# Performance work log

Measured on AMD Instinct MI355X. Metric: run time of the kernel, lower is better.

Reference implementation:

```python
import jax, jax.numpy as jnp
import numpy as np
from jax import lax

B, C, N = 8, 3, 65536
NUM_POINTS = 1024


def setup_inputs() -> dict:
    key = jax.random.key(0)
    points = jax.random.normal(key, (B, C, N), dtype=jnp.float32)
    return {"points": points}


def furthest_point_sampling(xyz, num_points):
    # xyz: (B, N, 3) -> indices (B, num_points), int32
    b, n, _ = xyz.shape
    init_idx = jnp.zeros((b,), dtype=jnp.int32)  # CUDA FPS seeds with index 0
    init_dists = jnp.full((b, n), 1e10, dtype=xyz.dtype)

    def step(carry, _):
        dists, last_idx = carry
        last_pt = jnp.take_along_axis(xyz, last_idx[:, None, None], axis=1)  # (B,1,3)
        d = jnp.sum(jnp.square(xyz - last_pt), axis=-1)  # (B,N) squared dist to newest pt
        dists = jnp.minimum(dists, d)
        nxt = jnp.argmax(dists, axis=-1).astype(jnp.int32)
        return (dists, nxt), nxt

    (_, _), rest = lax.scan(step, (init_dists, init_idx), None, length=num_points - 1)
    # rest: (num_points-1, B) -> (B, num_points)
    idx = jnp.concatenate([init_idx[None, :], rest], axis=0).T
    return idx


def reference(points):
    # points: (B, 3, N), channels-first as in the torch module
    xyz = jnp.transpose(points, (0, 2, 1))  # (B, N, 3)
    idx = furthest_point_sampling(xyz, NUM_POINTS)  # (B, num_points)
    # fps_gather_by_index: gather along point axis of (B, 3, N)
    new_points = jnp.take_along_axis(points, idx[:, None, :], axis=2)  # (B, 3, num_points)
    return new_points
```

## Files before the change

kernel.cpp:

```cpp
#include <hip/hip_runtime.h>


namespace {

constexpr int kB = 8;
constexpr int kN = 65536;
constexpr int kNP = 1024;
constexpr int kPB = 16;
constexpr int kThreads = 256;
constexpr int kPPT = kN / (kPB * kThreads);
constexpr int kGrp = kPPT / 4;
constexpr int kWaves = kThreads / 64;
constexpr int kRgn = 16;

__device__ __forceinline__ unsigned long long shfl_xor_u64(unsigned long long v, int off) {
  return (unsigned long long)__shfl_xor((long long)v, off, 64);
}

__device__ __forceinline__ unsigned long long u64max(unsigned long long a,
                                                     unsigned long long b) {
  return a > b ? a : b;
}

__global__ __launch_bounds__(kThreads) void fps_kernel(const float* __restrict__ pts,
                                                       float* __restrict__ out,
                                                       unsigned long long* __restrict__ slots) {
  const int batch = blockIdx.x & 7;
  const int slice = blockIdx.x >> 3;
  const int tid = threadIdx.x;
  const int lane = tid & 63;
  const int wave = tid >> 6;

  const float* __restrict__ xb = pts + (size_t)batch * 3 * kN;
  const float* __restrict__ yb = xb + kN;
  const float* __restrict__ zb = xb + 2 * kN;

  __shared__ unsigned long long s_wkey[kWaves];
  __shared__ unsigned s_win[2];
  __shared__ int s_hist[kNP];

  if (tid == 0) {
    s_win[0] = 0xFFFFFFFFu;
    s_win[1] = 0xFFFFFFFFu;
  }

  const int sbase = slice * (kThreads * kPPT);
  const int base0 = sbase + tid * 4;
  float px[kPPT], py[kPPT], pz[kPPT], dist[kPPT];
#pragma unroll
  for (int g = 0; g < kGrp; ++g) {
    const int base = base0 + g * (kThreads * 4);
    const float4 vx = *reinterpret_cast<const float4*>(xb + base);
    const float4 vy = *reinterpret_cast<const float4*>(yb + base);
    const float4 vz = *reinterpret_cast<const float4*>(zb + base);
    px[g * 4 + 0] = vx.x; px[g * 4 + 1] = vx.y; px[g * 4 + 2] = vx.z; px[g * 4 + 3] = vx.w;
    py[g * 4 + 0] = vy.x; py[g * 4 + 1] = vy.y; py[g * 4 + 2] = vy.z; py[g * 4 + 3] = vy.w;
    pz[g * 4 + 0] = vz.x; pz[g * 4 + 1] = vz.y; pz[g * 4 + 2] = vz.z; pz[g * 4 + 3] = vz.w;
  }
#pragma unroll
  for (int k = 0; k < kPPT; ++k) dist[k] = 1e10f;

  float qx = xb[0], qy = yb[0], qz = zb[0];

  unsigned long long* const sb = slots + (size_t)batch * kRgn * kPB;

  for (int it = 1; it < kNP; ++it) {
    float bd = -1.0f;
    int bi = 0;
#pragma unroll
    for (int g = 0; g < kGrp; ++g) {
#pragma unroll
      for (int j = 0; j < 4; ++j) {
        const int k = g * 4 + j;
        const float dx = px[k] - qx;
        const float dy = py[k] - qy;
        const float dz = pz[k] - qz;
        const float ss =
            __fadd_rn(__fadd_rn(__fmul_rn(dx, dx), __fmul_rn(dy, dy)), __fmul_rn(dz, dz));
        const float nd = fminf(dist[k], ss);
        dist[k] = nd;
        if (nd > bd) {
          bd = nd;
          bi = base0 + g * (kThreads * 4) + j;
        }
      }
    }

    unsigned long long key = ((unsigned long long)__float_as_uint(bd) << 32) |
                             ((unsigned long long)(0xFFFFu - (unsigned)bi) << 16) |
                             (unsigned long long)(unsigned)it;

#pragma unroll
    for (int off = 32; off > 0; off >>= 1) {
      key = u64max(key, shfl_xor_u64(key, off));
    }
    if (lane == 0) s_wkey[wave] = key;
    __syncthreads();

    int wi;
    if (wave == 0) {
      unsigned long long bk = s_wkey[lane & (kWaves - 1)];
#pragma unroll
      for (int off = 1; off < kWaves; off <<= 1) {
        bk = u64max(bk, shfl_xor_u64(bk, off));
      }

      unsigned long long* const rgn = sb + (size_t)(it & (kRgn - 1)) * kPB;
      if (lane == 0) {
        __hip_atomic_store(rgn + slice, bk, __ATOMIC_RELAXED, __HIP_MEMORY_SCOPE_AGENT);
      }

      unsigned long long w;
      for (;;) {
        w = __hip_atomic_load(rgn + (lane & (kPB - 1)), __ATOMIC_RELAXED,
                              __HIP_MEMORY_SCOPE_AGENT);
        if (__all((unsigned)(w & 0xFFFFull) == (unsigned)it)) break;
      }
#pragma unroll
      for (int off = 1; off < kPB; off <<= 1) {
        w = u64max(w, shfl_xor_u64(w, off));
      }
      wi = (int)(0xFFFFu - ((unsigned)(w >> 16) & 0xFFFFu));
      if (lane == 0) {
        s_hist[it] = wi;
        __hip_atomic_store(&s_win[it & 1], ((unsigned)wi << 16) | (unsigned)it,
                           __ATOMIC_RELAXED, __HIP_MEMORY_SCOPE_WORKGROUP);
      }
    } else {
      unsigned v;
      do {
        v = __hip_atomic_load(&s_win[it & 1], __ATOMIC_RELAXED, __HIP_MEMORY_SCOPE_WORKGROUP);
      } while ((v & 0xFFFFu) != (unsigned)it);
      wi = (int)(v >> 16);
    }

    const int wiu = __builtin_amdgcn_readfirstlane(wi);
    qx = xb[wiu];
    qy = yb[wiu];
    qz = zb[wiu];
  }

  __syncthreads();

  if (slice == 0) {
    float* __restrict__ ob = out + (size_t)batch * 3 * kNP;
    for (int j = tid; j < kNP; j += kThreads) {
      const int id = (j == 0) ? 0 : s_hist[j];
      ob[j] = xb[id];
      ob[kNP + j] = yb[id];
      ob[2 * kNP + j] = zb[id];
    }
  }
}

}

extern "C" void kernel_launch(void* const* d_in, const int* in_sizes, int n_in,
                              void* d_out, int out_size, void* d_ws, size_t ws_size,
                              hipStream_t stream) {
  (void)in_sizes;
  (void)n_in;
  (void)out_size;
  (void)ws_size;
  const float* pts = (const float*)d_in[0];
  float* out = (float*)d_out;
  unsigned long long* slots = (unsigned long long*)d_ws;
  fps_kernel<<<dim3(kB * kPB), dim3(kThreads), 0, stream>>>(pts, out, slots);
}
```

Measured before the change: 1.721 ms.

## Publish winner coordinates through exchange slots and use DPP wave reductions

```diff
diff --git a/kernel.cpp b/kernel.cpp
--- a/kernel.cpp
+++ b/kernel.cpp
@@ -12,14 +12,37 @@
 constexpr int kGrp = kPPT / 4;
 constexpr int kWaves = kThreads / 64;
 constexpr int kRgn = 16;
-
-__device__ __forceinline__ unsigned long long shfl_xor_u64(unsigned long long v, int off) {
-  return (unsigned long long)__shfl_xor((long long)v, off, 64);
-}
+constexpr int kRec = 4;
+constexpr int kWords = kPB * kRec;
 
 __device__ __forceinline__ unsigned long long u64max(unsigned long long a,
                                                      unsigned long long b) {
   return a > b ? a : b;
+}
+
+template <int CTRL>
+__device__ __forceinline__ unsigned long long dpp_u64_zero(unsigned long long v) {
+  const unsigned lo =
+      (unsigned)__builtin_amdgcn_update_dpp(0, (int)(unsigned)v, CTRL, 0xf, 0xf, false);
+  const unsigned hi =
+      (unsigned)__builtin_amdgcn_update_dpp(0, (int)(unsigned)(v >> 32), CTRL, 0xf, 0xf, false);
+  return ((unsigned long long)hi << 32) | lo;
+}
+
+__device__ __forceinline__ unsigned long long wave_max_u64(unsigned long long v) {
+  v = u64max(v, dpp_u64_zero<0x111>(v));
+  v = u64max(v, dpp_u64_zero<0x112>(v));
+  v = u64max(v, dpp_u64_zero<0x114>(v));
+  v = u64max(v, dpp_u64_zero<0x118>(v));
+  v = u64max(v, dpp_u64_zero<0x142>(v));
+  v = u64max(v, dpp_u64_zero<0x143>(v));
+  const unsigned lo = (unsigned)__builtin_amdgcn_readlane((int)(unsigned)v, 63);
+  const unsigned hi = (unsigned)__builtin_amdgcn_readlane((int)(unsigned)(v >> 32), 63);
+  return ((unsigned long long)hi << 32) | lo;
+}
+
+__device__ __forceinline__ unsigned long long shfl_u64(unsigned long long v, int src) {
+  return (unsigned long long)__shfl((long long)v, src, 64);
 }
 
 __global__ __launch_bounds__(kThreads) void fps_kernel(const float* __restrict__ pts,
@@ -36,6 +59,8 @@
   const float* __restrict__ zb = xb + 2 * kN;
 
   __shared__ unsigned long long s_wkey[kWaves];
+  __shared__ float s_wc[kWaves][3];
+  __shared__ float s_q[3];
   __shared__ unsigned s_win[2];
   __shared__ int s_hist[kNP];
 
@@ -62,10 +87,12 @@
 
   float qx = xb[0], qy = yb[0], qz = zb[0];
 
-  unsigned long long* const sb = slots + (size_t)batch * kRgn * kPB;
+  unsigned long long* const sb = slots + (size_t)batch * kRgn * kWords;
 
   for (int it = 1; it < kNP; ++it) {
-    float bd = -1.0f;
+    const unsigned tag = (unsigned)it;
+
+    float bd = -1.0f, bx = 0.f, by = 0.f, bz = 0.f;
     int bi = 0;
 #pragma unroll
     for (int g = 0; g < kGrp; ++g) {
@@ -82,62 +109,76 @@
         if (nd > bd) {
           bd = nd;
           bi = base0 + g * (kThreads * 4) + j;
+          bx = px[k]; by = py[k]; bz = pz[k];
         }
       }
     }
 
-    unsigned long long key = ((unsigned long long)__float_as_uint(bd) << 32) |
-                             ((unsigned long long)(0xFFFFu - (unsigned)bi) << 16) |
-                             (unsigned long long)(unsigned)it;
-
-#pragma unroll
-    for (int off = 32; off > 0; off >>= 1) {
-      key = u64max(key, shfl_xor_u64(key, off));
-    }
-    if (lane == 0) s_wkey[wave] = key;
+    const unsigned long long mykey = ((unsigned long long)__float_as_uint(bd) << 32) |
+                                     ((unsigned long long)(0xFFFFu - (unsigned)bi) << 16) |
+                                     (unsigned long long)tag;
+
+    const unsigned long long wk = wave_max_u64(mykey);
+    if (mykey == wk) {
+      s_wc[wave][0] = bx;
+      s_wc[wave][1] = by;
+      s_wc[wave][2] = bz;
+    }
+    if (lane == 0) s_wkey[wave] = wk;
     __syncthreads();
 
-    int wi;
     if (wave == 0) {
-      unsigned long long bk = s_wkey[lane & (kWaves - 1)];
-#pragma unroll
-      for (int off = 1; off < kWaves; off <<= 1) {
-        bk = u64max(bk, shfl_xor_u64(bk, off));
-      }
-
-      unsigned long long* const rgn = sb + (size_t)(it & (kRgn - 1)) * kPB;
+      const unsigned long long lk = s_wkey[lane & (kWaves - 1)];
+      const unsigned long long bk = wave_max_u64(lk);
+      const unsigned long long m = __ballot(lane < kWaves && lk == bk);
+      const int winwave = (int)(__ffsll((long long)m) - 1);
+
+      unsigned long long* const rgn = sb + (size_t)(it & (kRgn - 1)) * kWords;
       if (lane == 0) {
-        __hip_atomic_store(rgn + slice, bk, __ATOMIC_RELAXED, __HIP_MEMORY_SCOPE_AGENT);
+        const float wx = s_wc[winwave][0];
+        const float wy = s_wc[winwave][1];
+        const float wz = s_wc[winwave][2];
+        unsigned long long* const my = rgn + slice * kRec;
+        __hip_atomic_store(my + 0, bk, __ATOMIC_RELAXED, __HIP_MEMORY_SCOPE_AGENT);
+        __hip_atomic_store(my + 1, ((unsigned long long)__float_as_uint(wx) << 32) | tag,
+                           __ATOMIC_RELAXED, __HIP_MEMORY_SCOPE_AGENT);
+        __hip_atomic_store(my + 2, ((unsigned long long)__float_as_uint(wy) << 32) | tag,
+                           __ATOMIC_RELAXED, __HIP_MEMORY_SCOPE_AGENT);
+        __hip_atomic_store(my + 3, ((unsigned long long)__float_as_uint(wz) << 32) | tag,
+                           __ATOMIC_RELAXED, __HIP_MEMORY_SCOPE_AGENT);
       }
 
       unsigned long long w;
       for (;;) {
-        w = __hip_atomic_load(rgn + (lane & (kPB - 1)), __ATOMIC_RELAXED,
-                              __HIP_MEMORY_SCOPE_AGENT);
-        if (__all((unsigned)(w & 0xFFFFull) == (unsigned)it)) break;
-      }
-#pragma unroll
-      for (int off = 1; off < kPB; off <<= 1) {
-        w = u64max(w, shfl_xor_u64(w, off));
-      }
-      wi = (int)(0xFFFFu - ((unsigned)(w >> 16) & 0xFFFFu));
+        w = __hip_atomic_load(rgn + lane, __ATOMIC_RELAXED, __HIP_MEMORY_SCOPE_AGENT);
+        if (__all((unsigned)(w & 0xFFFFull) == tag)) break;
+      }
+
+      const unsigned long long kw = ((lane & 3) == 0) ? w : 0ull;
+      const unsigned long long mx = wave_max_u64(kw);
+      const unsigned long long skey = shfl_u64(w, lane & ~3);
+      const int wrd = lane & 3;
+      if (skey == mx && wrd != 0) {
+        s_q[wrd - 1] = __uint_as_float((unsigned)(w >> 32));
+      }
+      const int wi = (int)(0xFFFFu - ((unsigned)(mx >> 16) & 0xFFFFu));
       if (lane == 0) {
         s_hist[it] = wi;
-        __hip_atomic_store(&s_win[it & 1], ((unsigned)wi << 16) | (unsigned)it,
-                           __ATOMIC_RELAXED, __HIP_MEMORY_SCOPE_WORKGROUP);
-      }
+        __hip_atomic_store(&s_win[it & 1], ((unsigned)wi << 16) | tag, __ATOMIC_RELEASE,
+                           __HIP_MEMORY_SCOPE_WORKGROUP);
+      }
+      qx = s_q[0];
+      qy = s_q[1];
+      qz = s_q[2];
     } else {
       unsigned v;
       do {
-        v = __hip_atomic_load(&s_win[it & 1], __ATOMIC_RELAXED, __HIP_MEMORY_SCOPE_WORKGROUP);
-      } while ((v & 0xFFFFu) != (unsigned)it);
-      wi = (int)(v >> 16);
-    }
-
-    const int wiu = __builtin_amdgcn_readfirstlane(wi);
-    qx = xb[wiu];
-    qy = yb[wiu];
-    qz = zb[wiu];
+        v = __hip_atomic_load(&s_win[it & 1], __ATOMIC_ACQUIRE, __HIP_MEMORY_SCOPE_WORKGROUP);
+      } while ((v & 0xFFFFu) != tag);
+      qx = s_q[0];
+      qy = s_q[1];
+      qz = s_q[2];
+    }
   }
 
   __syncthreads();
```

Measured after the change: 3.796 ms. +120.6%, slower.
